# Performance work log

Measured on AMD Instinct MI355X. Metric: run time of the kernel, lower is better.

Reference implementation:

```python
import jax, jax.numpy as jnp
import numpy as np

PARAM = 10.0
EPS = 1e-10

def delu(x):
    # delu_feature_map: param*relu(x) + (exp(param*min(x,0)) - 1) + 1
    return PARAM * jax.nn.relu(x) + jnp.expm1(PARAM * jnp.minimum(x, 0.0)) + 1.0

def conv1x1(x, w, b):
    # x: (B,C,H,W), w: (O,C), b: (O,)
    return jnp.einsum('oc,bchw->bohw', w, x) + b[None, :, None, None]

def conv3x3(x, w, b):
    # x: (B,C,H,W), w: (O,C,3,3)
    y = jax.lax.conv_general_dilated(x, w, window_strides=(1, 1), padding='SAME',
                                     dimension_numbers=('NCHW', 'OIHW', 'NCHW'))
    return y + b[None, :, None, None]

def setup_inputs() -> dict:
    key = jax.random.key(0)
    B, C, H, W = 4, 256, 128, 128
    ks = jax.random.split(key, 20)
    s = 0.05
    d = {
        'x1': jax.random.normal(ks[0], (B, C, H, W), jnp.float32),
        'x2': jax.random.normal(ks[1], (B, C, H, W), jnp.float32),
        'wq1': jax.random.normal(ks[2], (C, C), jnp.float32) * s,
        'bq1': jax.random.normal(ks[3], (C,), jnp.float32) * s,
        'wk1': jax.random.normal(ks[4], (C, C), jnp.float32) * s,
        'bk1': jax.random.normal(ks[5], (C,), jnp.float32) * s,
        'wv1': jax.random.normal(ks[6], (C, C), jnp.float32) * s,
        'bv1': jax.random.normal(ks[7], (C,), jnp.float32) * s,
        'wq2': jax.random.normal(ks[8], (C, C), jnp.float32) * s,
        'bq2': jax.random.normal(ks[9], (C,), jnp.float32) * s,
        'wk2': jax.random.normal(ks[10], (C, C), jnp.float32) * s,
        'bk2': jax.random.normal(ks[11], (C,), jnp.float32) * s,
        'wv2': jax.random.normal(ks[12], (C, C), jnp.float32) * s,
        'bv2': jax.random.normal(ks[13], (C,), jnp.float32) * s,
        'wd1': jax.random.normal(ks[14], (C, C), jnp.float32) * s,
        'bd1': jax.random.normal(ks[15], (C,), jnp.float32) * s,
        'wd3': jax.random.normal(ks[16], (C, C, 3, 3), jnp.float32) * s,
        'bd3': jax.random.normal(ks[17], (C,), jnp.float32) * s,
        'gamma1': jax.random.normal(ks[18], (1,), jnp.float32) * 0.5,
        'gamma2': jax.random.normal(ks[19], (1,), jnp.float32) * 0.5,
    }
    return d

def reference(x1, x2, wq1, bq1, wk1, bk1, wv1, bv1, wq2, bq2, wk2, bk2,
              wv2, bv2, wd1, bd1, wd3, bd3, gamma1, gamma2):
    B, C, H, W = x1.shape
    N = H * W
    # QKV projections (1x1 convs), flattened to (B,C,N). delu is elementwise,
    # so applying it on (B,C,N) equals the permute/delu/permute in torch.
    q1 = delu(conv1x1(x1, wq1, bq1).reshape(B, C, N))
    k1 = delu(conv1x1(x1, wk1, bk1).reshape(B, C, N))
    v1 = conv1x1(x1, wv1, bv1).reshape(B, C, N)
    q2 = delu(conv1x1(x2, wq2, bq2).reshape(B, C, N))
    k2 = delu(conv1x1(x2, wk2, bk2).reshape(B, C, N))
    v2 = conv1x1(x2, wv2, bv2).reshape(B, C, N)

    # energy: (B,C,C) cross-kernel matrices
    energy1 = jnp.einsum('bmn,bcn->bmc', q1, k2)
    energy2 = jnp.einsum('bmn,bcn->bmc', q2, k1)

    KV1 = k1 * v1  # (B,C,N)
    KV2 = k2 * v2

    # norm: 1 / (sum_{m,c} energy[b,m,c] * k[b,c,n] + eps) -> (B,N)
    esum1 = energy1.sum(axis=1)  # (B,C)
    esum2 = energy2.sum(axis=1)
    norm1 = 1.0 / (jnp.einsum('bc,bcn->bn', esum1, k2) + EPS)
    norm2 = 1.0 / (jnp.einsum('bc,bcn->bn', esum2, k1) + EPS)

    # einsum('bmc,bcn,bn->bcn') factorizes: sum over m hits only energy
    att1 = (esum1[:, :, None] * KV1 * norm1[:, None, :]).reshape(B, C, H, W)
    att2 = (esum2[:, :, None] * KV2 * norm2[:, None, :]).reshape(B, C, H, W)

    out1 = att1 + conv1x1(x1, wd1, bd1) + conv3x3(x1, wd3, bd3)
    out2 = att2 + conv1x1(x2, wd1, bd1) + conv3x3(x2, wd3, bd3)
    out1 = x1 + gamma1[0] * out1
    out2 = x2 + gamma2[0] * out2
    return (out1, out2)
```

## Files before the change

### kernel.cpp

```cpp
#include <hip/hip_runtime.h>
#include <stdint.h>

#define Bn 4
#define Cn 256
#define Hn 128
#define Wn 128
#define Nn 16384
#define EPSn 1e-10f

typedef unsigned short u16;
typedef __attribute__((ext_vector_type(8))) short short8;
typedef __attribute__((ext_vector_type(4))) short short4v;
typedef __attribute__((ext_vector_type(4))) float f32x4;

#define GLOAD_LDS16(g, l)                                                        \
    __builtin_amdgcn_global_load_lds(                                            \
        (const __attribute__((address_space(1))) unsigned int*)(const void*)(g), \
        (__attribute__((address_space(3))) unsigned int*)(void*)(l), 16, 0, 0)

__device__ __forceinline__ float bf2f(u16 u) {
    union { float f; uint32_t i; } v; v.i = ((uint32_t)u) << 16; return v.f;
}
__device__ __forceinline__ u16 f2bf(float f) {
    union { float f; uint32_t i; } v; v.f = f;
    uint32_t r = v.i + 0x7FFFu + ((v.i >> 16) & 1u);
    return (u16)(r >> 16);
}
__device__ __forceinline__ float delu_f(float x) {
    return x >= 0.f ? fmaf(10.f, x, 1.f) : __expf(10.f * x);
}

__global__ void prep_kernel(const float* __restrict__ wq1, const float* __restrict__ wk1,
                            const float* __restrict__ wv1,
                            const float* __restrict__ wq2, const float* __restrict__ wk2,
                            const float* __restrict__ wv2,
                            const float* __restrict__ wd1, const float* __restrict__ wd3,
                            const float* __restrict__ bd1, const float* __restrict__ bd3,
                            const float* __restrict__ gamma1, const float* __restrict__ gamma2,
                            u16* __restrict__ wq1p, u16* __restrict__ wk1p, u16* __restrict__ wv1p,
                            u16* __restrict__ wq2p, u16* __restrict__ wk2p, u16* __restrict__ wv2p,
                            u16* __restrict__ wallp1, u16* __restrict__ wallp2,
                            float* __restrict__ bfused)
{
    int idx = blockIdx.x * 256 + threadIdx.x;
    int o = idx >> 8, c = idx & 255;
    if (idx < 256) bfused[idx] = bd1[idx] + bd3[idx];
    int s = o >> 6, mf = (o >> 4) & 3, lr = o & 15;
    int kc = c >> 5, lk = (c >> 3) & 3, j = c & 7;
    int poff = ((kc * 4 + s) * 4 + mf) * 512 + (lk * 16 + lr) * 8 + j;
    wq1p[poff] = f2bf(wq1[idx]);
    wk1p[poff] = f2bf(wk1[idx]);
    wv1p[poff] = f2bf(wv1[idx]);
    wq2p[poff] = f2bf(wq2[idx]);
    wk2p[poff] = f2bf(wk2[idx]);
    wv2p[poff] = f2bf(wv2[idx]);
    float wd1v = wd1[idx];
    float inv1 = 1.f / gamma1[0];
    float inv2 = 1.f / gamma2[0];
    float diag = (o == c) ? 1.f : 0.f;
    #pragma unroll
    for (int tap = 0; tap < 9; ++tap) {
        float w = wd3[idx * 9 + tap] + (tap == 4 ? wd1v : 0.f);
        wallp1[tap * 65536 + poff] = f2bf(w + (tap == 4 ? diag * inv1 : 0.f));
        wallp2[tap * 65536 + poff] = f2bf(w + (tap == 4 ? diag * inv2 : 0.f));
    }
}

__global__ void transpose_kernel(const float* __restrict__ x, u16* __restrict__ xT)
{
    __shared__ __align__(16) u16 tl[64][72];
    int t = threadIdx.x;
    int n0 = blockIdx.x * 64, c0 = blockIdx.y * 64, b = blockIdx.z;
    int cl = t >> 4, nl = (t & 15) * 4;
    #pragma unroll
    for (int pc = 0; pc < 4; ++pc) {
        int c = pc * 16 + cl;
        float4 v = *(const float4*)&x[((size_t)(b * Cn + c0 + c)) * Nn + n0 + nl];
        tl[nl + 0][c] = f2bf(v.x);
        tl[nl + 1][c] = f2bf(v.y);
        tl[nl + 2][c] = f2bf(v.z);
        tl[nl + 3][c] = f2bf(v.w);
    }
    __syncthreads();
    #pragma unroll
    for (int ps = 0; ps < 2; ++ps) {
        int id = ps * 256 + t;
        int nr = id >> 3, cc = (id & 7) * 8;
        short8 v = *(const short8*)&tl[nr][cc];
        *(short8*)&xT[((size_t)(b * Nn + n0 + nr)) * 256 + c0 + cc] = v;
    }
}

__global__ __launch_bounds__(256, 2) void qkv_kernel(
    const u16* __restrict__ xT,
    const u16* __restrict__ wqp, const u16* __restrict__ wkp, const u16* __restrict__ wvp,
    const float* __restrict__ bq, const float* __restrict__ bk, const float* __restrict__ bv,
    u16* __restrict__ kout, u16* __restrict__ kvout, float* __restrict__ qsum)
{
    __shared__ __align__(16) u16 Bt[2 * 4096];
    int t = threadIdx.x;
    int nb = blockIdx.x, mb = blockIdx.y, b = blockIdx.z;
    int lane = t & 63, wid = t >> 6;
    int wm = wid >> 1, wn = wid & 1;
    int lr = lane & 15, lk = lane >> 4;
    int s = mb * 2 + wm;

    f32x4 zf = {0.f, 0.f, 0.f, 0.f};
    f32x4 accq[4][4], acck[4][4], accv[4][4];
    #pragma unroll
    for (int i = 0; i < 4; ++i)
        #pragma unroll
        for (int j = 0; j < 4; ++j) { accq[i][j] = zf; acck[i][j] = zf; accv[i][j] = zf; }

    int colp = lane >> 2, chp = (lane & 3) * 8;
    auto STAGE = [&](int bufi, int kc) {
        #pragma unroll
        for (int i = 0; i < 2; ++i) {
            int col0 = (wid * 2 + i) * 16;
            const u16* g = xT + ((size_t)(b * Nn + nb * 128 + col0 + colp)) * 256 + kc * 32 + chp;
            GLOAD_LDS16(g, &Bt[bufi * 4096 + col0 * 32]);
        }
    };

    STAGE(0, 0);
    __syncthreads();

    #pragma unroll 2
    for (int kc = 0; kc < 8; ++kc) {
        int cur = kc & 1;
        if (kc < 7) STAGE(cur ^ 1, kc + 1);
        int abase = ((kc * 4 + s) * 4) * 512 + lane * 8;
        short8 bf[4];
        #pragma unroll
        for (int nf = 0; nf < 4; ++nf)
            bf[nf] = *(const short8*)&Bt[cur * 4096 + (wn * 64 + nf * 16 + lr) * 32 + lk * 8];
        #pragma unroll
        for (int mf = 0; mf < 4; ++mf) {
            short8 aq = *(const short8*)&wqp[abase + mf * 512];
            short8 ak = *(const short8*)&wkp[abase + mf * 512];
            short8 av = *(const short8*)&wvp[abase + mf * 512];
            #pragma unroll
            for (int nf = 0; nf < 4; ++nf) {
                accq[mf][nf] = __builtin_amdgcn_mfma_f32_16x16x32_bf16(aq, bf[nf], accq[mf][nf], 0, 0, 0);
                acck[mf][nf] = __builtin_amdgcn_mfma_f32_16x16x32_bf16(ak, bf[nf], acck[mf][nf], 0, 0, 0);
                accv[mf][nf] = __builtin_amdgcn_mfma_f32_16x16x32_bf16(av, bf[nf], accv[mf][nf], 0, 0, 0);
            }
        }
        __syncthreads();
    }

    float qs[4] = {0.f, 0.f, 0.f, 0.f};
    #pragma unroll
    for (int mf = 0; mf < 4; ++mf) {
        #pragma unroll
        for (int r = 0; r < 4; ++r) {
            int o = mb * 128 + wm * 64 + mf * 16 + lk * 4 + r;
            float bqv = bq[o], bkv = bk[o], bvv = bv[o];
            #pragma unroll
            for (int nf = 0; nf < 4; ++nf) {
                int n = nb * 128 + wn * 64 + nf * 16 + lr;
                size_t idx = ((size_t)(b * Cn + o)) * Nn + n;
                float qv = delu_f(accq[mf][nf][r] + bqv);
                qs[nf] += qv;
                float kk = delu_f(acck[mf][nf][r] + bkv);
                kout[idx] = f2bf(kk);
                float vv = accv[mf][nf][r] + bvv;
                kvout[idx] = f2bf(kk * vv);
            }
        }
    }
    #pragma unroll
    for (int nf = 0; nf < 4; ++nf) {
        float sgl = qs[nf];
        sgl += __shfl_xor(sgl, 16);
        sgl += __shfl_xor(sgl, 32);
        if (lk == 0)
            atomicAdd(&qsum[b * Nn + nb * 128 + wn * 64 + nf * 16 + lr], sgl);
    }
}

__global__ void esum_kernel(const u16* __restrict__ k, const float* __restrict__ qsum,
                            float* __restrict__ esum)
{
    int c = blockIdx.x, b = blockIdx.y, t = threadIdx.x;
    const u16* kr = k + ((size_t)(b * Cn + c)) * Nn;
    const float* qr = qsum + b * Nn;
    float s = 0.f;
    for (int i = t * 8; i < Nn; i += 2048) {
        short8 kv = *(const short8*)&kr[i];
        #pragma unroll
        for (int j = 0; j < 8; ++j) s = fmaf(bf2f((u16)kv[j]), qr[i + j], s);
    }
    #pragma unroll
    for (int m = 32; m; m >>= 1) s += __shfl_xor(s, m);
    __shared__ float red[4];
    if ((t & 63) == 0) red[t >> 6] = s;
    __syncthreads();
    if (t == 0) esum[b * Cn + c] = red[0] + red[1] + red[2] + red[3];
}

__global__ void norm_kernel(const u16* __restrict__ k, const float* __restrict__ esum,
                            float* __restrict__ nrm)
{
    __shared__ float es[256];
    int t = threadIdx.x, b = blockIdx.y;
    es[t] = esum[b * Cn + t];
    __syncthreads();
    int n = blockIdx.x * 256 + t;
    const u16* kb = k + (size_t)b * Cn * Nn + n;
    float a = 0.f;
    #pragma unroll 8
    for (int c = 0; c < 256; ++c)
        a = fmaf(es[c], bf2f(kb[(size_t)c * Nn]), a);
    nrm[b * Nn + n] = 1.f / (a + EPSn);
}

#define BROW 130
#define BSZ  (4 * BROW * 32)

__global__ __launch_bounds__(256, 2) void conv_att_kernel(
    const u16* __restrict__ xT,
    const u16* __restrict__ wallp, const float* __restrict__ bfused,
    const u16* __restrict__ kv, const float* __restrict__ esum,
    const float* __restrict__ nrm, const float* __restrict__ gamma,
    float* __restrict__ out)
{
    __shared__ __align__(16) u16 Bl[2 * BSZ];
    int t = threadIdx.x;
    int lin = (blockIdx.z * 64 + blockIdx.y) * 2 + blockIdx.x;
    int wg = (lin & 7) * 64 + (lin >> 3);
    int mb = wg & 1, yp = (wg >> 1) & 63, b = wg >> 7;
    int ybase = yp * 2;
    int lane = t & 63, wid = t >> 6;
    int wm = wid >> 1, wy = wid & 1;
    int lr = lane & 15, lk = lane >> 4;
    int s = mb * 2 + wm;

    f32x4 zf = {0.f, 0.f, 0.f, 0.f};
    f32x4 acc[4][8];
    #pragma unroll
    for (int i = 0; i < 4; ++i)
        #pragma unroll
        for (int j = 0; j < 8; ++j) acc[i][j] = zf;

    if (t < 64) {
        int buf = t >> 5, rr = (t >> 3) & 3, pos = (t & 4) ? 129 : 0, chq = t & 3;
        short8 z = {0, 0, 0, 0, 0, 0, 0, 0};
        *(short8*)&Bl[buf * BSZ + (rr * BROW + pos) * 32 + chq * 8] = z;
    }

    int colp = lane >> 2, chp = (lane & 3) * 8;
    auto STAGE = [&](int bufi, int kc) {
        #pragma unroll
        for (int i = 0; i < 8; ++i) {
            int ch = wid * 8 + i;
            int hy = ch >> 3, sx = ch & 7;
            int yy = ybase + hy - 1;
            int base = bufi * BSZ + (hy * BROW + 1 + sx * 16) * 32;
            if (yy < 0 || yy >= Hn) {
                short8 z = {0, 0, 0, 0, 0, 0, 0, 0};
                *(short8*)&Bl[base + lane * 8] = z;
            } else {
                const u16* g = xT + ((size_t)(b * Nn + yy * Wn + sx * 16 + colp)) * 256
                                  + kc * 32 + chp;
                GLOAD_LDS16(g, &Bl[base]);
            }
        }
    };

    STAGE(0, 0);
    __syncthreads();

    #pragma unroll 2
    for (int kc = 0; kc < 8; ++kc) {
        int cur = kc & 1;
        if (kc < 7) STAGE(cur ^ 1, kc + 1);
        int cb = cur * BSZ;
        int abase = ((kc * 4 + s) * 4) * 512 + lane * 8;
        #pragma unroll
        for (int dy = 0; dy < 3; ++dy) {
            #pragma unroll
            for (int dx = 0; dx < 3; ++dx) {
                short8 bf[8];
                #pragma unroll
                for (int nf = 0; nf < 8; ++nf)
                    bf[nf] = *(const short8*)&Bl[cb + ((wy + dy) * BROW + nf * 16 + lr + dx) * 32 + lk * 8];
                const u16* ap = wallp + (dy * 3 + dx) * 65536 + abase;
                #pragma unroll
                for (int mf = 0; mf < 4; ++mf) {
                    short8 af = *(const short8*)&ap[mf * 512];
                    #pragma unroll
                    for (int nf = 0; nf < 8; ++nf)
                        acc[mf][nf] = __builtin_amdgcn_mfma_f32_16x16x32_bf16(af, bf[nf], acc[mf][nf], 0, 0, 0);
                }
            }
        }
        __syncthreads();
    }

    float g = gamma[0];
    int nrow = (ybase + wy) * Wn;
    float nr8[8];
    #pragma unroll
    for (int nf = 0; nf < 8; ++nf)
        nr8[nf] = nrm[b * Nn + nrow + nf * 16 + lr];
    #pragma unroll
    for (int mf = 0; mf < 4; ++mf) {
        #pragma unroll
        for (int r = 0; r < 4; ++r) {
            int o = mb * 128 + wm * 64 + mf * 16 + lk * 4 + r;
            float es_o = esum[b * Cn + o];
            float bf_o = bfused[o];
            size_t rowbase = ((size_t)(b * Cn + o)) * Nn + nrow;
            #pragma unroll
            for (int nf = 0; nf < 8; ++nf) {
                size_t idx = rowbase + nf * 16 + lr;
                float att = es_o * bf2f(kv[idx]) * nr8[nf];
                out[idx] = g * (acc[mf][nf][r] + bf_o + att);
            }
        }
    }
}

extern "C" void kernel_launch(void* const* d_in, const int* in_sizes, int n_in,
                              void* d_out, int out_size, void* d_ws, size_t ws_size,
                              hipStream_t stream)
{
    const float* x1  = (const float*)d_in[0];
    const float* x2  = (const float*)d_in[1];
    const float* wq1 = (const float*)d_in[2];
    const float* bq1 = (const float*)d_in[3];
    const float* wk1 = (const float*)d_in[4];
    const float* bk1 = (const float*)d_in[5];
    const float* wv1 = (const float*)d_in[6];
    const float* bv1 = (const float*)d_in[7];
    const float* wq2 = (const float*)d_in[8];
    const float* bq2 = (const float*)d_in[9];
    const float* wk2 = (const float*)d_in[10];
    const float* bk2 = (const float*)d_in[11];
    const float* wv2 = (const float*)d_in[12];
    const float* bv2 = (const float*)d_in[13];
    const float* wd1 = (const float*)d_in[14];
    const float* bd1 = (const float*)d_in[15];
    const float* wd3 = (const float*)d_in[16];
    const float* bd3 = (const float*)d_in[17];
    const float* gamma1 = (const float*)d_in[18];
    const float* gamma2 = (const float*)d_in[19];

    char* ws = (char*)d_ws;
    size_t off = 0;
    auto alloc = [&](size_t bytes) { char* p = ws + off; off += (bytes + 255) & ~(size_t)255; return p; };

    u16* xT1    = (u16*)alloc((size_t)Bn * Nn * Cn * 2);
    u16* xT2    = (u16*)alloc((size_t)Bn * Nn * Cn * 2);
    u16* k1     = (u16*)alloc((size_t)Bn * Cn * Nn * 2);
    u16* k2     = (u16*)alloc((size_t)Bn * Cn * Nn * 2);
    u16* kv2    = (u16*)alloc((size_t)Bn * Cn * Nn * 2);
    u16* wallp1 = (u16*)alloc((size_t)9 * 65536 * 2);
    u16* wallp2 = (u16*)alloc((size_t)9 * 65536 * 2);
    u16* wq1p   = (u16*)alloc(65536 * 2);
    u16* wk1p   = (u16*)alloc(65536 * 2);
    u16* wv1p   = (u16*)alloc(65536 * 2);
    u16* wq2p   = (u16*)alloc(65536 * 2);
    u16* wk2p   = (u16*)alloc(65536 * 2);
    u16* wv2p   = (u16*)alloc(65536 * 2);
    float* qsum1 = (float*)alloc(Bn * Nn * 4);
    float* qsum2 = (float*)alloc(Bn * Nn * 4);
    float* esum1 = (float*)alloc(Bn * Cn * 4);
    float* esum2 = (float*)alloc(Bn * Cn * 4);
    float* norm1 = (float*)alloc(Bn * Nn * 4);
    float* norm2 = (float*)alloc(Bn * Nn * 4);
    float* bfused = (float*)alloc(Cn * 4);

    float* out1 = (float*)d_out;
    float* out2 = out1 + (size_t)Bn * Cn * Nn;
    u16* kv1 = (u16*)out2;

    hipMemsetAsync(qsum1, 0, Bn * Nn * 4, stream);
    hipMemsetAsync(qsum2, 0, Bn * Nn * 4, stream);

    prep_kernel<<<dim3(256), dim3(256), 0, stream>>>(wq1, wk1, wv1, wq2, wk2, wv2, wd1, wd3,
                                                     bd1, bd3, gamma1, gamma2,
                                                     wq1p, wk1p, wv1p, wq2p, wk2p, wv2p,
                                                     wallp1, wallp2, bfused);
    transpose_kernel<<<dim3(256, 4, 4), 256, 0, stream>>>(x1, xT1);
    transpose_kernel<<<dim3(256, 4, 4), 256, 0, stream>>>(x2, xT2);
    qkv_kernel<<<dim3(128, 2, 4), 256, 0, stream>>>(xT1, wq1p, wk1p, wv1p, bq1, bk1, bv1,
                                                    k1, kv1, qsum1);
    qkv_kernel<<<dim3(128, 2, 4), 256, 0, stream>>>(xT2, wq2p, wk2p, wv2p, bq2, bk2, bv2,
                                                    k2, kv2, qsum2);
    esum_kernel<<<dim3(256, 4), 256, 0, stream>>>(k2, qsum1, esum1);
    esum_kernel<<<dim3(256, 4), 256, 0, stream>>>(k1, qsum2, esum2);
    norm_kernel<<<dim3(64, 4), 256, 0, stream>>>(k2, esum1, norm1);
    norm_kernel<<<dim3(64, 4), 256, 0, stream>>>(k1, esum2, norm2);
    conv_att_kernel<<<dim3(2, 64, 4), 256, 0, stream>>>(xT1, wallp1, bfused, kv1,
                                                        esum1, norm1, gamma1, out1);
    conv_att_kernel<<<dim3(2, 64, 4), 256, 0, stream>>>(xT2, wallp2, bfused, kv2,
                                                        esum2, norm2, gamma2, out2);
}
```

Before: 390.9 us.

## Split V projection into own kernel, shrink conv tile, preload weights, add setprio

New measurement: 392.1 us. No clear change (+0.3%).

```diff
diff --git a/kernel.cpp b/kernel.cpp
--- a/kernel.cpp
+++ b/kernel.cpp
@@ -17,6 +17,8 @@
     __builtin_amdgcn_global_load_lds(                                            \
         (const __attribute__((address_space(1))) unsigned int*)(const void*)(g), \
         (__attribute__((address_space(3))) unsigned int*)(void*)(l), 16, 0, 0)
+
+#define MFMA16(a, b, c) __builtin_amdgcn_mfma_f32_16x16x32_bf16(a, b, c, 0, 0, 0)
 
 __device__ __forceinline__ float bf2f(u16 u) {
     union { float f; uint32_t i; } v; v.i = ((uint32_t)u) << 16; return v.f;
@@ -91,11 +93,11 @@
     }
 }
 
-__global__ __launch_bounds__(256, 2) void qkv_kernel(
+__global__ __launch_bounds__(256, 2) void qk_kernel(
     const u16* __restrict__ xT,
-    const u16* __restrict__ wqp, const u16* __restrict__ wkp, const u16* __restrict__ wvp,
-    const float* __restrict__ bq, const float* __restrict__ bk, const float* __restrict__ bv,
-    u16* __restrict__ kout, u16* __restrict__ kvout, float* __restrict__ qsum)
+    const u16* __restrict__ wqp, const u16* __restrict__ wkp,
+    const float* __restrict__ bq, const float* __restrict__ bk,
+    u16* __restrict__ kout, float* __restrict__ qsum)
 {
     __shared__ __align__(16) u16 Bt[2 * 4096];
     int t = threadIdx.x;
@@ -106,11 +108,11 @@
     int s = mb * 2 + wm;
 
     f32x4 zf = {0.f, 0.f, 0.f, 0.f};
-    f32x4 accq[4][4], acck[4][4], accv[4][4];
+    f32x4 accq[4][4], acck[4][4];
     #pragma unroll
     for (int i = 0; i < 4; ++i)
         #pragma unroll
-        for (int j = 0; j < 4; ++j) { accq[i][j] = zf; acck[i][j] = zf; accv[i][j] = zf; }
+        for (int j = 0; j < 4; ++j) { accq[i][j] = zf; acck[i][j] = zf; }
 
     int colp = lane >> 2, chp = (lane & 3) * 8;
     auto STAGE = [&](int bufi, int kc) {
@@ -125,27 +127,30 @@
     STAGE(0, 0);
     __syncthreads();
 
-    #pragma unroll 2
     for (int kc = 0; kc < 8; ++kc) {
         int cur = kc & 1;
+        int abase = ((kc * 4 + s) * 4) * 512 + lane * 8;
+        short8 aq[4], ak[4];
+        #pragma unroll
+        for (int mf = 0; mf < 4; ++mf) {
+            aq[mf] = *(const short8*)&wqp[abase + mf * 512];
+            ak[mf] = *(const short8*)&wkp[abase + mf * 512];
+        }
         if (kc < 7) STAGE(cur ^ 1, kc + 1);
-        int abase = ((kc * 4 + s) * 4) * 512 + lane * 8;
         short8 bf[4];
         #pragma unroll
         for (int nf = 0; nf < 4; ++nf)
             bf[nf] = *(const short8*)&Bt[cur * 4096 + (wn * 64 + nf * 16 + lr) * 32 + lk * 8];
+        __builtin_amdgcn_s_setprio(1);
         #pragma unroll
         for (int mf = 0; mf < 4; ++mf) {
-            short8 aq = *(const short8*)&wqp[abase + mf * 512];
-            short8 ak = *(const short8*)&wkp[abase + mf * 512];
-            short8 av = *(const short8*)&wvp[abase + mf * 512];
             #pragma unroll
             for (int nf = 0; nf < 4; ++nf) {
-                accq[mf][nf] = __builtin_amdgcn_mfma_f32_16x16x32_bf16(aq, bf[nf], accq[mf][nf], 0, 0, 0);
-                acck[mf][nf] = __builtin_amdgcn_mfma_f32_16x16x32_bf16(ak, bf[nf], acck[mf][nf], 0, 0, 0);
-                accv[mf][nf] = __builtin_amdgcn_mfma_f32_16x16x32_bf16(av, bf[nf], accv[mf][nf], 0, 0, 0);
-            }
-        }
+                accq[mf][nf] = MFMA16(aq[mf], bf[nf], accq[mf][nf]);
+                acck[mf][nf] = MFMA16(ak[mf], bf[nf], acck[mf][nf]);
+            }
+        }
+        __builtin_amdgcn_s_setprio(0);
         __syncthreads();
     }
 
@@ -155,17 +160,15 @@
         #pragma unroll
         for (int r = 0; r < 4; ++r) {
             int o = mb * 128 + wm * 64 + mf * 16 + lk * 4 + r;
-            float bqv = bq[o], bkv = bk[o], bvv = bv[o];
+            float bqv = bq[o], bkv = bk[o];
             #pragma unroll
             for (int nf = 0; nf < 4; ++nf) {
                 int n = nb * 128 + wn * 64 + nf * 16 + lr;
                 size_t idx = ((size_t)(b * Cn + o)) * Nn + n;
                 float qv = delu_f(accq[mf][nf][r] + bqv);
                 qs[nf] += qv;
-                float kk = delu_f(acck[mf][nf][r] + bkv);
-                kout[idx] = f2bf(kk);
-                float vv = accv[mf][nf][r] + bvv;
-                kvout[idx] = f2bf(kk * vv);
+                float kkv = delu_f(acck[mf][nf][r] + bkv);
+                kout[idx] = f2bf(kkv);
             }
         }
     }
@@ -176,6 +179,75 @@
         sgl += __shfl_xor(sgl, 32);
         if (lk == 0)
             atomicAdd(&qsum[b * Nn + nb * 128 + wn * 64 + nf * 16 + lr], sgl);
+    }
+}
+
+__global__ __launch_bounds__(256) void v_kernel(
+    const u16* __restrict__ xT, const u16* __restrict__ wvp,
+    const float* __restrict__ bv, u16* __restrict__ vout)
+{
+    __shared__ __align__(16) u16 Bt[2 * 4096];
+    int t = threadIdx.x;
+    int nb = blockIdx.x, mb = blockIdx.y, b = blockIdx.z;
+    int lane = t & 63, wid = t >> 6;
+    int wm = wid >> 1, wn = wid & 1;
+    int lr = lane & 15, lk = lane >> 4;
+    int s = mb * 2 + wm;
+
+    f32x4 zf = {0.f, 0.f, 0.f, 0.f};
+    f32x4 accv[4][4];
+    #pragma unroll
+    for (int i = 0; i < 4; ++i)
+        #pragma unroll
+        for (int j = 0; j < 4; ++j) accv[i][j] = zf;
+
+    int colp = lane >> 2, chp = (lane & 3) * 8;
+    auto STAGE = [&](int bufi, int kc) {
+        #pragma unroll
+        for (int i = 0; i < 2; ++i) {
+            int col0 = (wid * 2 + i) * 16;
+            const u16* g = xT + ((size_t)(b * Nn + nb * 128 + col0 + colp)) * 256 + kc * 32 + chp;
+            GLOAD_LDS16(g, &Bt[bufi * 4096 + col0 * 32]);
+        }
+    };
+
+    STAGE(0, 0);
+    __syncthreads();
+
+    for (int kc = 0; kc < 8; ++kc) {
+        int cur = kc & 1;
+        int abase = ((kc * 4 + s) * 4) * 512 + lane * 8;
+        short8 av[4];
+        #pragma unroll
+        for (int mf = 0; mf < 4; ++mf)
+            av[mf] = *(const short8*)&wvp[abase + mf * 512];
+        if (kc < 7) STAGE(cur ^ 1, kc + 1);
+        short8 bf[4];
+        #pragma unroll
+        for (int nf = 0; nf < 4; ++nf)
+            bf[nf] = *(const short8*)&Bt[cur * 4096 + (wn * 64 + nf * 16 + lr) * 32 + lk * 8];
+        __builtin_amdgcn_s_setprio(1);
+        #pragma unroll
+        for (int mf = 0; mf < 4; ++mf)
+            #pragma unroll
+            for (int nf = 0; nf < 4; ++nf)
+                accv[mf][nf] = MFMA16(av[mf], bf[nf], accv[mf][nf]);
+        __builtin_amdgcn_s_setprio(0);
+        __syncthreads();
+    }
+
+    #pragma unroll
+    for (int mf = 0; mf < 4; ++mf) {
+        #pragma unroll
+        for (int r = 0; r < 4; ++r) {
+            int o = mb * 128 + wm * 64 + mf * 16 + lk * 4 + r;
+            float bvv = bv[o];
+            #pragma unroll
+            for (int nf = 0; nf < 4; ++nf) {
+                int n = nb * 128 + wn * 64 + nf * 16 + lr;
+                vout[((size_t)(b * Cn + o)) * Nn + n] = f2bf(accv[mf][nf][r] + bvv);
+            }
+        }
     }
 }
 
@@ -215,55 +287,55 @@
     nrm[b * Nn + n] = 1.f / (a + EPSn);
 }
 
-#define BROW 130
-#define BSZ  (4 * BROW * 32)
+#define BSZ3 (3 * 130 * 32)
 
 __global__ __launch_bounds__(256, 2) void conv_att_kernel(
     const u16* __restrict__ xT,
     const u16* __restrict__ wallp, const float* __restrict__ bfused,
-    const u16* __restrict__ kv, const float* __restrict__ esum,
-    const float* __restrict__ nrm, const float* __restrict__ gamma,
-    float* __restrict__ out)
-{
-    __shared__ __align__(16) u16 Bl[2 * BSZ];
+    const u16* __restrict__ kk, const u16* __restrict__ vv,
+    const float* __restrict__ esum, const float* __restrict__ nrm,
+    const float* __restrict__ gamma, float* __restrict__ out)
+{
+    __shared__ __align__(16) u16 Bl[2 * BSZ3];
     int t = threadIdx.x;
-    int lin = (blockIdx.z * 64 + blockIdx.y) * 2 + blockIdx.x;
-    int wg = (lin & 7) * 64 + (lin >> 3);
-    int mb = wg & 1, yp = (wg >> 1) & 63, b = wg >> 7;
-    int ybase = yp * 2;
+    int lin = (blockIdx.z * 128 + blockIdx.y) * 2 + blockIdx.x;
+    int wg = (lin & 7) * 128 + (lin >> 3);
+    int mb = wg & 1, y = (wg >> 1) & 127, b = wg >> 8;
     int lane = t & 63, wid = t >> 6;
-    int wm = wid >> 1, wy = wid & 1;
+    int wm = wid >> 1, wp = wid & 1;
     int lr = lane & 15, lk = lane >> 4;
     int s = mb * 2 + wm;
 
     f32x4 zf = {0.f, 0.f, 0.f, 0.f};
-    f32x4 acc[4][8];
+    f32x4 acc[4][4];
     #pragma unroll
     for (int i = 0; i < 4; ++i)
         #pragma unroll
-        for (int j = 0; j < 8; ++j) acc[i][j] = zf;
-
-    if (t < 64) {
-        int buf = t >> 5, rr = (t >> 3) & 3, pos = (t & 4) ? 129 : 0, chq = t & 3;
+        for (int j = 0; j < 4; ++j) acc[i][j] = zf;
+
+    if (t < 48) {
+        int q = t & 3, slot = t >> 2;
+        int buf = slot > 5 ? 1 : 0, r6 = slot - buf * 6;
+        int row = r6 >> 1, pos = (r6 & 1) ? 129 : 0;
         short8 z = {0, 0, 0, 0, 0, 0, 0, 0};
-        *(short8*)&Bl[buf * BSZ + (rr * BROW + pos) * 32 + chq * 8] = z;
+        *(short8*)&Bl[buf * BSZ3 + (row * 130 + pos) * 32 + q * 8] = z;
     }
 
     int colp = lane >> 2, chp = (lane & 3) * 8;
     auto STAGE = [&](int bufi, int kc) {
         #pragma unroll
-        for (int i = 0; i < 8; ++i) {
-            int ch = wid * 8 + i;
-            int hy = ch >> 3, sx = ch & 7;
-            int yy = ybase + hy - 1;
-            int base = bufi * BSZ + (hy * BROW + 1 + sx * 16) * 32;
+        for (int i = 0; i < 6; ++i) {
+            int run = wid * 6 + i;
+            int hy = run >> 3, sx = run & 7;
+            int yy = y + hy - 1;
+            int dst = bufi * BSZ3 + (hy * 130 + 1 + sx * 16) * 32;
             if (yy < 0 || yy >= Hn) {
                 short8 z = {0, 0, 0, 0, 0, 0, 0, 0};
-                *(short8*)&Bl[base + lane * 8] = z;
+                *(short8*)&Bl[dst + lane * 8] = z;
             } else {
                 const u16* g = xT + ((size_t)(b * Nn + yy * Wn + sx * 16 + colp)) * 256
                                   + kc * 32 + chp;
-                GLOAD_LDS16(g, &Bl[base]);
+                GLOAD_LDS16(g, &Bl[dst]);
             }
         }
     };
@@ -271,39 +343,46 @@
     STAGE(0, 0);
     __syncthreads();
 
-    #pragma unroll 2
     for (int kc = 0; kc < 8; ++kc) {
         int cur = kc & 1;
+        int abase = ((kc * 4 + s) * 4) * 512 + lane * 8;
+        short8 af[9][4];
+        #pragma unroll
+        for (int tap = 0; tap < 9; ++tap)
+            #pragma unroll
+            for (int mf = 0; mf < 4; ++mf)
+                af[tap][mf] = *(const short8*)&wallp[tap * 65536 + abase + mf * 512];
         if (kc < 7) STAGE(cur ^ 1, kc + 1);
-        int cb = cur * BSZ;
-        int abase = ((kc * 4 + s) * 4) * 512 + lane * 8;
+        int cb = cur * BSZ3;
         #pragma unroll
         for (int dy = 0; dy < 3; ++dy) {
             #pragma unroll
             for (int dx = 0; dx < 3; ++dx) {
-                short8 bf[8];
+                int tap = dy * 3 + dx;
+                short8 bf[4];
                 #pragma unroll
-                for (int nf = 0; nf < 8; ++nf)
-                    bf[nf] = *(const short8*)&Bl[cb + ((wy + dy) * BROW + nf * 16 + lr + dx) * 32 + lk * 8];
-                const u16* ap = wallp + (dy * 3 + dx) * 65536 + abase;
+                for (int nf = 0; nf < 4; ++nf)
+                    bf[nf] = *(const short8*)&Bl[cb + (dy * 130 + wp * 64 + nf * 16 + lr + dx) * 32 + lk * 8];
+                __builtin_amdgcn_s_setprio(1);
                 #pragma unroll
                 for (int mf = 0; mf < 4; ++mf) {
-                    short8 af = *(const short8*)&ap[mf * 512];
-                    #pragma unroll
-                    for (int nf = 0; nf < 8; ++nf)
-                        acc[mf][nf] = __builtin_amdgcn_mfma_f32_16x16x32_bf16(af, bf[nf], acc[mf][nf], 0, 0, 0);
+                    acc[mf][0] = MFMA16(af[tap][mf], bf[0], acc[mf][0]);
+                    acc[mf][1] = MFMA16(af[tap][mf], bf[1], acc[mf][1]);
+                    acc[mf][2] = MFMA16(af[tap][mf], bf[2], acc[mf][2]);
+                    acc[mf][3] = MFMA16(af[tap][mf], bf[3], acc[mf][3]);
                 }
+                __builtin_amdgcn_s_setprio(0);
             }
         }
         __syncthreads();
     }
 
     float g = gamma[0];
-    int nrow = (ybase + wy) * Wn;
-    float nr8[8];
-    #pragma unroll
-    for (int nf = 0; nf < 8; ++nf)
-        nr8[nf] = nrm[b * Nn + nrow + nf * 16 + lr];
+    int nbase = y * Wn + wp * 64;
+    float nr4[4];
+    #pragma unroll
+    for (int nf = 0; nf < 4; ++nf)
+        nr4[nf] = nrm[b * Nn + nbase + nf * 16 + lr];
     #pragma unroll
     for (int mf = 0; mf < 4; ++mf) {
         #pragma unroll
@@ -311,11 +390,11 @@
             int o = mb * 128 + wm * 64 + mf * 16 + lk * 4 + r;
             float es_o = esum[b * Cn + o];
             float bf_o = bfused[o];
-            size_t rowbase = ((size_t)(b * Cn + o)) * Nn + nrow;
-            #pragma unroll
-            for (int nf = 0; nf < 8; ++nf) {
+            size_t rowbase = ((size_t)(b * Cn + o)) * Nn + nbase;
+            #pragma unroll
+            for (int nf = 0; nf < 4; ++nf) {
                 size_t idx = rowbase + nf * 16 + lr;
-                float att = es_o * bf2f(kv[idx]) * nr8[nf];
+                float att = es_o * bf2f(kk[idx]) * bf2f(vv[idx]) * nr4[nf];
                 out[idx] = g * (acc[mf][nf][r] + bf_o + att);
             }
         }
@@ -355,7 +434,7 @@
     u16* xT2    = (u16*)alloc((size_t)Bn * Nn * Cn * 2);
     u16* k1     = (u16*)alloc((size_t)Bn * Cn * Nn * 2);
     u16* k2     = (u16*)alloc((size_t)Bn * Cn * Nn * 2);
-    u16* kv2    = (u16*)alloc((size_t)Bn * Cn * Nn * 2);
+    u16* v2     = (u16*)alloc((size_t)Bn * Cn * Nn * 2);
     u16* wallp1 = (u16*)alloc((size_t)9 * 65536 * 2);
     u16* wallp2 = (u16*)alloc((size_t)9 * 65536 * 2);
     u16* wq1p   = (u16*)alloc(65536 * 2);
@@ -374,7 +453,7 @@
 
     float* out1 = (float*)d_out;
     float* out2 = out1 + (size_t)Bn * Cn * Nn;
-    u16* kv1 = (u16*)out2;
+    u16* v1 = (u16*)out2;
 
     hipMemsetAsync(qsum1, 0, Bn * Nn * 4, stream);
     hipMemsetAsync(qsum2, 0, Bn * Nn * 4, stream);
@@ -385,16 +464,16 @@
                                                      wallp1, wallp2, bfused);
     transpose_kernel<<<dim3(256, 4, 4), 256, 0, stream>>>(x1, xT1);
     transpose_kernel<<<dim3(256, 4, 4), 256, 0, stream>>>(x2, xT2);
-    qkv_kernel<<<dim3(128, 2, 4), 256, 0, stream>>>(xT1, wq1p, wk1p, wv1p, bq1, bk1, bv1,
-                                                    k1, kv1, qsum1);
-    qkv_kernel<<<dim3(128, 2, 4), 256, 0, stream>>>(xT2, wq2p, wk2p, wv2p, bq2, bk2, bv2,
-                                                    k2, kv2, qsum2);
+    qk_kernel<<<dim3(128, 2, 4), 256, 0, stream>>>(xT1, wq1p, wk1p, bq1, bk1, k1, qsum1);
+    qk_kernel<<<dim3(128, 2, 4), 256, 0, stream>>>(xT2, wq2p, wk2p, bq2, bk2, k2, qsum2);
+    v_kernel<<<dim3(128, 2, 4), 256, 0, stream>>>(xT1, wv1p, bv1, v1);
+    v_kernel<<<dim3(128, 2, 4), 256, 0, stream>>>(xT2, wv2p, bv2, v2);
     esum_kernel<<<dim3(256, 4), 256, 0, stream>>>(k2, qsum1, esum1);
     esum_kernel<<<dim3(256, 4), 256, 0, stream>>>(k1, qsum2, esum2);
     norm_kernel<<<dim3(64, 4), 256, 0, stream>>>(k2, esum1, norm1);
     norm_kernel<<<dim3(64, 4), 256, 0, stream>>>(k1, esum2, norm2);
-    conv_att_kernel<<<dim3(2, 64, 4), 256, 0, stream>>>(xT1, wallp1, bfused, kv1,
-                                                        esum1, norm1, gamma1, out1);
-    conv_att_kernel<<<dim3(2, 64, 4), 256, 0, stream>>>(xT2, wallp2, bfused, kv2,
-                                                        esum2, norm2, gamma2, out2);
-}
+    conv_att_kernel<<<dim3(2, 128, 4), 256, 0, stream>>>(xT1, wallp1, bfused, k1, v1,
+                                                         esum1, norm1, gamma1, out1);
+    conv_att_kernel<<<dim3(2, 128, 4), 256, 0, stream>>>(xT2, wallp2, bfused, k2, v2,
+                                                         esum2, norm2, gamma2, out2);
+}
```

## Batch both images per launch and enlarge conv tile with register weight prefetch

Applied to the files above, without the earlier changes.

Result: faster. 357.2 us (-8.6%).

```diff
diff --git a/kernel.cpp b/kernel.cpp
--- a/kernel.cpp
+++ b/kernel.cpp
@@ -17,6 +17,8 @@
     __builtin_amdgcn_global_load_lds(                                            \
         (const __attribute__((address_space(1))) unsigned int*)(const void*)(g), \
         (__attribute__((address_space(3))) unsigned int*)(void*)(l), 16, 0, 0)
+
+#define MFMA16(a, b, c) __builtin_amdgcn_mfma_f32_16x16x32_bf16(a, b, c, 0, 0, 0)
 
 __device__ __forceinline__ float bf2f(u16 u) {
     union { float f; uint32_t i; } v; v.i = ((uint32_t)u) << 16; return v.f;
@@ -66,11 +68,15 @@
     }
 }
 
-__global__ void transpose_kernel(const float* __restrict__ x, u16* __restrict__ xT)
+__global__ void transpose_kernel(const float* __restrict__ x1, const float* __restrict__ x2,
+                                 u16* __restrict__ xT1, u16* __restrict__ xT2)
 {
     __shared__ __align__(16) u16 tl[64][72];
     int t = threadIdx.x;
-    int n0 = blockIdx.x * 64, c0 = blockIdx.y * 64, b = blockIdx.z;
+    int z = blockIdx.z, img = z >> 2, b = z & 3;
+    const float* x = img ? x2 : x1;
+    u16* xT = img ? xT2 : xT1;
+    int n0 = blockIdx.x * 64, c0 = blockIdx.y * 64;
     int cl = t >> 4, nl = (t & 15) * 4;
     #pragma unroll
     for (int pc = 0; pc < 4; ++pc) {
@@ -92,14 +98,30 @@
 }
 
 __global__ __launch_bounds__(256, 2) void qkv_kernel(
-    const u16* __restrict__ xT,
-    const u16* __restrict__ wqp, const u16* __restrict__ wkp, const u16* __restrict__ wvp,
-    const float* __restrict__ bq, const float* __restrict__ bk, const float* __restrict__ bv,
-    u16* __restrict__ kout, u16* __restrict__ kvout, float* __restrict__ qsum)
+    const u16* __restrict__ xT1, const u16* __restrict__ xT2,
+    const u16* __restrict__ wq1p, const u16* __restrict__ wk1p, const u16* __restrict__ wv1p,
+    const u16* __restrict__ wq2p, const u16* __restrict__ wk2p, const u16* __restrict__ wv2p,
+    const float* __restrict__ bq1, const float* __restrict__ bk1, const float* __restrict__ bv1,
+    const float* __restrict__ bq2, const float* __restrict__ bk2, const float* __restrict__ bv2,
+    u16* __restrict__ k1, u16* __restrict__ k2,
+    u16* __restrict__ kv1, u16* __restrict__ kv2,
+    float* __restrict__ qsum1, float* __restrict__ qsum2)
 {
     __shared__ __align__(16) u16 Bt[2 * 4096];
     int t = threadIdx.x;
-    int nb = blockIdx.x, mb = blockIdx.y, b = blockIdx.z;
+    int nb = blockIdx.x, mb = blockIdx.y;
+    int z = blockIdx.z, img = z >> 2, b = z & 3;
+    const u16* xT  = img ? xT2  : xT1;
+    const u16* wqp = img ? wq2p : wq1p;
+    const u16* wkp = img ? wk2p : wk1p;
+    const u16* wvp = img ? wv2p : wv1p;
+    const float* bq = img ? bq2 : bq1;
+    const float* bk = img ? bk2 : bk1;
+    const float* bv = img ? bv2 : bv1;
+    u16* kout  = img ? k2  : k1;
+    u16* kvout = img ? kv2 : kv1;
+    float* qsum = img ? qsum2 : qsum1;
+
     int lane = t & 63, wid = t >> 6;
     int wm = wid >> 1, wn = wid & 1;
     int lr = lane & 15, lk = lane >> 4;
@@ -125,7 +147,6 @@
     STAGE(0, 0);
     __syncthreads();
 
-    #pragma unroll 2
     for (int kc = 0; kc < 8; ++kc) {
         int cur = kc & 1;
         if (kc < 7) STAGE(cur ^ 1, kc + 1);
@@ -139,12 +160,14 @@
             short8 aq = *(const short8*)&wqp[abase + mf * 512];
             short8 ak = *(const short8*)&wkp[abase + mf * 512];
             short8 av = *(const short8*)&wvp[abase + mf * 512];
+            __builtin_amdgcn_s_setprio(1);
             #pragma unroll
             for (int nf = 0; nf < 4; ++nf) {
-                accq[mf][nf] = __builtin_amdgcn_mfma_f32_16x16x32_bf16(aq, bf[nf], accq[mf][nf], 0, 0, 0);
-                acck[mf][nf] = __builtin_amdgcn_mfma_f32_16x16x32_bf16(ak, bf[nf], acck[mf][nf], 0, 0, 0);
-                accv[mf][nf] = __builtin_amdgcn_mfma_f32_16x16x32_bf16(av, bf[nf], accv[mf][nf], 0, 0, 0);
-            }
+                accq[mf][nf] = MFMA16(aq, bf[nf], accq[mf][nf]);
+                acck[mf][nf] = MFMA16(ak, bf[nf], acck[mf][nf]);
+                accv[mf][nf] = MFMA16(av, bf[nf], accv[mf][nf]);
+            }
+            __builtin_amdgcn_s_setprio(0);
         }
         __syncthreads();
     }
@@ -179,10 +202,14 @@
     }
 }
 
-__global__ void esum_kernel(const u16* __restrict__ k, const float* __restrict__ qsum,
-                            float* __restrict__ esum)
-{
-    int c = blockIdx.x, b = blockIdx.y, t = threadIdx.x;
+__global__ void esum_kernel(const u16* __restrict__ k1, const u16* __restrict__ k2,
+                            const float* __restrict__ qsum1, const float* __restrict__ qsum2,
+                            float* __restrict__ esum1, float* __restrict__ esum2)
+{
+    int c = blockIdx.x, b = blockIdx.y, pair = blockIdx.z, t = threadIdx.x;
+    const u16* k = pair ? k1 : k2;
+    const float* qsum = pair ? qsum2 : qsum1;
+    float* esum = pair ? esum2 : esum1;
     const u16* kr = k + ((size_t)(b * Cn + c)) * Nn;
     const float* qr = qsum + b * Nn;
     float s = 0.f;
@@ -199,11 +226,15 @@
     if (t == 0) esum[b * Cn + c] = red[0] + red[1] + red[2] + red[3];
 }
 
-__global__ void norm_kernel(const u16* __restrict__ k, const float* __restrict__ esum,
-                            float* __restrict__ nrm)
+__global__ void norm_kernel(const u16* __restrict__ k1, const u16* __restrict__ k2,
+                            const float* __restrict__ esum1, const float* __restrict__ esum2,
+                            float* __restrict__ norm1, float* __restrict__ norm2)
 {
     __shared__ float es[256];
-    int t = threadIdx.x, b = blockIdx.y;
+    int t = threadIdx.x, b = blockIdx.y, pair = blockIdx.z;
+    const u16* k = pair ? k1 : k2;
+    const float* esum = pair ? esum2 : esum1;
+    float* nrm = pair ? norm2 : norm1;
     es[t] = esum[b * Cn + t];
     __syncthreads();
     int n = blockIdx.x * 256 + t;
@@ -215,24 +246,22 @@
     nrm[b * Nn + n] = 1.f / (a + EPSn);
 }
 
-#define BROW 130
-#define BSZ  (4 * BROW * 32)
-
-__global__ __launch_bounds__(256, 2) void conv_att_kernel(
+#define BSZ6 (6 * 130 * 32)
+
+__global__ __launch_bounds__(512, 2) void conv_att_kernel(
     const u16* __restrict__ xT,
     const u16* __restrict__ wallp, const float* __restrict__ bfused,
     const u16* __restrict__ kv, const float* __restrict__ esum,
     const float* __restrict__ nrm, const float* __restrict__ gamma,
     float* __restrict__ out)
 {
-    __shared__ __align__(16) u16 Bl[2 * BSZ];
+    __shared__ __align__(16) u16 Bl[2 * BSZ6];
     int t = threadIdx.x;
-    int lin = (blockIdx.z * 64 + blockIdx.y) * 2 + blockIdx.x;
-    int wg = (lin & 7) * 64 + (lin >> 3);
-    int mb = wg & 1, yp = (wg >> 1) & 63, b = wg >> 7;
-    int ybase = yp * 2;
+    int lin = (blockIdx.z * 32 + blockIdx.y) * 2 + blockIdx.x;
+    int mb = lin & 1, b = (lin >> 1) & 3, ys = lin >> 3;
+    int ybase = ys * 4;
     int lane = t & 63, wid = t >> 6;
-    int wm = wid >> 1, wy = wid & 1;
+    int wm = wid & 1, wy = wid >> 1;
     int lr = lane & 15, lk = lane >> 4;
     int s = mb * 2 + wm;
 
@@ -243,27 +272,28 @@
         #pragma unroll
         for (int j = 0; j < 8; ++j) acc[i][j] = zf;
 
-    if (t < 64) {
-        int buf = t >> 5, rr = (t >> 3) & 3, pos = (t & 4) ? 129 : 0, chq = t & 3;
+    if (t < 96) {
+        int buf = t / 48, r = t % 48;
+        int row = r >> 3, pos = ((r >> 2) & 1) ? 129 : 0, q = r & 3;
         short8 z = {0, 0, 0, 0, 0, 0, 0, 0};
-        *(short8*)&Bl[buf * BSZ + (rr * BROW + pos) * 32 + chq * 8] = z;
+        *(short8*)&Bl[buf * BSZ6 + (row * 130 + pos) * 32 + q * 8] = z;
     }
 
     int colp = lane >> 2, chp = (lane & 3) * 8;
     auto STAGE = [&](int bufi, int kc) {
         #pragma unroll
-        for (int i = 0; i < 8; ++i) {
-            int ch = wid * 8 + i;
-            int hy = ch >> 3, sx = ch & 7;
+        for (int i = 0; i < 6; ++i) {
+            int run = wid * 6 + i;
+            int hy = run >> 3, sx = run & 7;
             int yy = ybase + hy - 1;
-            int base = bufi * BSZ + (hy * BROW + 1 + sx * 16) * 32;
+            int dst = bufi * BSZ6 + (hy * 130 + 1 + sx * 16) * 32;
             if (yy < 0 || yy >= Hn) {
                 short8 z = {0, 0, 0, 0, 0, 0, 0, 0};
-                *(short8*)&Bl[base + lane * 8] = z;
+                *(short8*)&Bl[dst + lane * 8] = z;
             } else {
                 const u16* g = xT + ((size_t)(b * Nn + yy * Wn + sx * 16 + colp)) * 256
                                   + kc * 32 + chp;
-                GLOAD_LDS16(g, &Bl[base]);
+                GLOAD_LDS16(g, &Bl[dst]);
             }
         }
     };
@@ -271,39 +301,50 @@
     STAGE(0, 0);
     __syncthreads();
 
-    #pragma unroll 2
     for (int kc = 0; kc < 8; ++kc) {
         int cur = kc & 1;
+        int abase = ((kc * 4 + s) * 4) * 512 + lane * 8;
+        short8 af[3][4];
+        #pragma unroll
+        for (int mf = 0; mf < 4; ++mf)
+            af[0][mf] = *(const short8*)&wallp[0 * 65536 + abase + mf * 512];
+        #pragma unroll
+        for (int mf = 0; mf < 4; ++mf)
+            af[1][mf] = *(const short8*)&wallp[1 * 65536 + abase + mf * 512];
         if (kc < 7) STAGE(cur ^ 1, kc + 1);
-        int cb = cur * BSZ;
-        int abase = ((kc * 4 + s) * 4) * 512 + lane * 8;
-        #pragma unroll
-        for (int dy = 0; dy < 3; ++dy) {
+        int cb = cur * BSZ6;
+        #pragma unroll
+        for (int tap = 0; tap < 9; ++tap) {
+            if (tap < 7) {
+                #pragma unroll
+                for (int mf = 0; mf < 4; ++mf)
+                    af[(tap + 2) % 3][mf] =
+                        *(const short8*)&wallp[(tap + 2) * 65536 + abase + mf * 512];
+            }
+            int dy = tap / 3, dx = tap % 3;
+            short8 bf[8];
             #pragma unroll
-            for (int dx = 0; dx < 3; ++dx) {
-                short8 bf[8];
+            for (int nf = 0; nf < 8; ++nf)
+                bf[nf] = *(const short8*)&Bl[cb + ((wy + dy) * 130 + nf * 16 + lr + dx) * 32 + lk * 8];
+            __builtin_amdgcn_s_setprio(1);
+            #pragma unroll
+            for (int mf = 0; mf < 4; ++mf) {
                 #pragma unroll
                 for (int nf = 0; nf < 8; ++nf)
-                    bf[nf] = *(const short8*)&Bl[cb + ((wy + dy) * BROW + nf * 16 + lr + dx) * 32 + lk * 8];
-                const u16* ap = wallp + (dy * 3 + dx) * 65536 + abase;
-                #pragma unroll
-                for (int mf = 0; mf < 4; ++mf) {
-                    short8 af = *(const short8*)&ap[mf * 512];
-                    #pragma unroll
-                    for (int nf = 0; nf < 8; ++nf)
-                        acc[mf][nf] = __builtin_amdgcn_mfma_f32_16x16x32_bf16(af, bf[nf], acc[mf][nf], 0, 0, 0);
-                }
-            }
+                    acc[mf][nf] = MFMA16(af[tap % 3][mf], bf[nf], acc[mf][nf]);
+            }
+            __builtin_amdgcn_s_setprio(0);
         }
         __syncthreads();
     }
 
     float g = gamma[0];
-    int nrow = (ybase + wy) * Wn;
+    int y = ybase + wy;
+    int nbase = y * Wn;
     float nr8[8];
     #pragma unroll
     for (int nf = 0; nf < 8; ++nf)
-        nr8[nf] = nrm[b * Nn + nrow + nf * 16 + lr];
+        nr8[nf] = nrm[b * Nn + nbase + nf * 16 + lr];
     #pragma unroll
     for (int mf = 0; mf < 4; ++mf) {
         #pragma unroll
@@ -311,7 +352,7 @@
             int o = mb * 128 + wm * 64 + mf * 16 + lk * 4 + r;
             float es_o = esum[b * Cn + o];
             float bf_o = bfused[o];
-            size_t rowbase = ((size_t)(b * Cn + o)) * Nn + nrow;
+            size_t rowbase = ((size_t)(b * Cn + o)) * Nn + nbase;
             #pragma unroll
             for (int nf = 0; nf < 8; ++nf) {
                 size_t idx = rowbase + nf * 16 + lr;
@@ -383,18 +424,15 @@
                                                      bd1, bd3, gamma1, gamma2,
                                                      wq1p, wk1p, wv1p, wq2p, wk2p, wv2p,
                                                      wallp1, wallp2, bfused);
-    transpose_kernel<<<dim3(256, 4, 4), 256, 0, stream>>>(x1, xT1);
-    transpose_kernel<<<dim3(256, 4, 4), 256, 0, stream>>>(x2, xT2);
-    qkv_kernel<<<dim3(128, 2, 4), 256, 0, stream>>>(xT1, wq1p, wk1p, wv1p, bq1, bk1, bv1,
-                                                    k1, kv1, qsum1);
-    qkv_kernel<<<dim3(128, 2, 4), 256, 0, stream>>>(xT2, wq2p, wk2p, wv2p, bq2, bk2, bv2,
-                                                    k2, kv2, qsum2);
-    esum_kernel<<<dim3(256, 4), 256, 0, stream>>>(k2, qsum1, esum1);
-    esum_kernel<<<dim3(256, 4), 256, 0, stream>>>(k1, qsum2, esum2);
-    norm_kernel<<<dim3(64, 4), 256, 0, stream>>>(k2, esum1, norm1);
-    norm_kernel<<<dim3(64, 4), 256, 0, stream>>>(k1, esum2, norm2);
-    conv_att_kernel<<<dim3(2, 64, 4), 256, 0, stream>>>(xT1, wallp1, bfused, kv1,
+    transpose_kernel<<<dim3(256, 4, 8), 256, 0, stream>>>(x1, x2, xT1, xT2);
+    qkv_kernel<<<dim3(128, 2, 8), 256, 0, stream>>>(xT1, xT2,
+                                                    wq1p, wk1p, wv1p, wq2p, wk2p, wv2p,
+                                                    bq1, bk1, bv1, bq2, bk2, bv2,
+                                                    k1, k2, kv1, kv2, qsum1, qsum2);
+    esum_kernel<<<dim3(256, 4, 2), 256, 0, stream>>>(k1, k2, qsum1, qsum2, esum1, esum2);
+    norm_kernel<<<dim3(64, 4, 2), 256, 0, stream>>>(k1, k2, esum1, esum2, norm1, norm2);
+    conv_att_kernel<<<dim3(2, 32, 4), 512, 0, stream>>>(xT1, wallp1, bfused, kv1,
                                                         esum1, norm1, gamma1, out1);
-    conv_att_kernel<<<dim3(2, 64, 4), 256, 0, stream>>>(xT2, wallp2, bfused, kv2,
+    conv_att_kernel<<<dim3(2, 32, 4), 512, 0, stream>>>(xT2, wallp2, bfused, kv2,
                                                         esum2, norm2, gamma2, out2);
 }
```
